# Kernel tuning notes

Hardware: AMD Instinct MI355X
Metric: run time of the kernel (lower is better)

Reference implementation:

```python
import jax, jax.numpy as jnp
import numpy as np

BIG = 1e9      # infinity sentinel used by the CUDA kernels
THRESH = 1e8   # 'min_val >= 1e8 -> invalid' cutoff
MAX_LEN = 512  # init kwarg max_length
BANDWIDTH = 0.2


def _dist(X, Y):
    # pairwise squared-euclidean: D[b,i,j] = sum_d (X[b,i,d]-Y[b,j,d])^2
    diff = X[:, :, None, :] - Y[:, None, :, :]  # [B,N,M,d]
    return jnp.sum(diff * diff, axis=-1)        # [B,N,M]


def _ldtw_dp(D, max_len, bandwidth):
    """Band-limited length-constrained DTW DP.
    Returns (min_vals[B], choices[max_len,B,N,M] int8, best_k[B]).
    choices[t] holds the step-(k=t+1) decisions at interior cells (i-1, j-1)."""
    B, N, M = D.shape
    ii = np.arange(1, N + 1)[:, None]
    jj = np.arange(1, M + 1)[None, :]
    band_bad = jnp.asarray((np.abs(ii - jj) > bandwidth * max(N, M)) & (bandwidth > 0))  # [N,M] static

    # prev_cost padded [B, N+2, M+2]; only (0,0) starts at 0, everything else BIG.
    prev0 = jnp.full((B, N + 2, M + 2), BIG, jnp.float32).at[:, 0, 0].set(0.0)

    def step(prev, _):
        # candidates for interior cells (i in 1..N, j in 1..M)
        cand = jnp.stack(
            [prev[:, 0:N, 0:M],       # diag  (choice 0)
             prev[:, 0:N, 1:M + 1],   # vert  (choice 1)
             prev[:, 1:N + 1, 0:M]],  # hori  (choice 2)
            axis=0)                    # [3,B,N,M]
        min_val = cand.min(axis=0)
        # argmin returns first minimum -> matches strict-less update order (diag,vert,hori)
        choice = jnp.argmin(cand, axis=0).astype(jnp.int8)
        valid = min_val < THRESH
        cost = jnp.where(band_bad[None] | ~valid, BIG, min_val + D)
        ch = jnp.where(valid & ~band_bad[None], choice, jnp.int8(-1))
        curr = jnp.full_like(prev, BIG).at[:, 1:N + 1, 1:M + 1].set(cost)
        return curr, (cost[:, N - 1, M - 1], ch)

    _, (final_costs, choices) = jax.lax.scan(step, prev0, None, length=max_len)
    # final_costs[t] is the cost of a length-(t+1) path ending at (N,M)
    mvl = max(N, M)
    valid_costs = final_costs[mvl - 1:]            # k in [mvl, max_len]
    min_vals = valid_costs.min(axis=0)             # [B]
    best_k = jnp.argmin(valid_costs, axis=0) + mvl # [B] (unused in fwd)
    return min_vals, choices, best_k


def setup_inputs() -> dict:
    key = jax.random.key(0)
    k1, k2 = jax.random.split(key)
    X = jax.random.normal(k1, (16, 256, 64), jnp.float32)
    Y = jax.random.normal(k2, (16, 256, 64), jnp.float32)
    return {"X": X, "Y": Y}


def reference(X, Y):
    D = _dist(X, Y)
    min_vals, _, _ = _ldtw_dp(D, MAX_LEN, BANDWIDTH)
    # original module returns (min_vals, None); the None carries no information
    return min_vals
```

## Files before the change

### kernel.cpp

```cpp
#include <hip/hip_runtime.h>

#define BIGV 1e9f
#define NPT 256

__device__ __forceinline__ int imin_of(int s){
    int a = s - 255; if (a < 0) a = 0;
    int c = s - 50;  c = (c > 0) ? (c >> 1) : 0;
    return (a > c) ? a : c;
}
__device__ __forceinline__ int imax_of(int s){
    int a = (s < 255) ? s : 255;
    int c = (s + 51) >> 1;
    return (a < c) ? a : c;
}

__device__ __forceinline__ int Wof(int g){
    int w = imin_of(8*g + 1) - 1;
    return (w < 0) ? 0 : ((w > 192) ? 192 : w);
}
__device__ __forceinline__ int wrow_of(int s){
    return (s == 0) ? 0 : Wof((s - 1) >> 3);
}

__device__ __forceinline__ float dpp_shr1(float x){
    return __int_as_float(__builtin_amdgcn_update_dpp(
        __float_as_int(BIGV), __float_as_int(x), 0x138 , 0xF, 0xF, false));
}
__device__ __forceinline__ float dpp_shl1(float x){
    return __int_as_float(__builtin_amdgcn_update_dpp(
        __float_as_int(BIGV), __float_as_int(x), 0x130 , 0xF, 0xF, false));
}

__device__ __forceinline__ float min3f(float a, float b, float c){
    float r;
    asm("v_min3_f32 %0, %1, %2, %3" : "=v"(r) : "v"(a), "v"(b), "v"(c));
    return r;
}

__global__ __launch_bounds__(256, 1) void ldtw_dist(const float* __restrict__ X,
                                                    const float* __restrict__ Y,
                                                    float* __restrict__ Dwin)
{
    __shared__ float4 Xs[80*17];
    __shared__ float4 Ys[80*17];
    __shared__ float nX[80], nY[80];
    __shared__ float Band[32*65];
    const int b  = blockIdx.x & 15;
    const int c  = blockIdx.x >> 4;
    const int s0 = c << 5;
    const int s1 = (s0 + 31 > 510) ? 510 : (s0 + 31);
    const int ilo = imin_of(s0), ihi = imax_of(s1);
    const int jlo = s0 - imax_of(s0), jhi = s1 - imin_of(s1);
    const int nx = ihi - ilo + 1, ny = jhi - jlo + 1;
    const int t = threadIdx.x;
    const float4* Xb = (const float4*)(X + (size_t)b * NPT * 64);
    const float4* Yb = (const float4*)(Y + (size_t)b * NPT * 64);

    for (int idx = t; idx < nx * 16; idx += 256){
        int r = idx >> 4, k = idx & 15;
        Xs[r*17 + k] = Xb[(ilo + r)*16 + k];
    }
    for (int idx = t; idx < ny * 16; idx += 256){
        int r = idx >> 4, k = idx & 15;
        Ys[r*17 + k] = Yb[(jlo + r)*16 + k];
    }
    __syncthreads();

    for (int r = t; r < nx + ny; r += 256){
        const float4* row = (r < nx) ? (Xs + r*17) : (Ys + (r - nx)*17);
        float acc = 0.f;
        #pragma unroll
        for (int k = 0; k < 16; ++k){
            float4 v = row[k];
            acc += v.x*v.x + v.y*v.y + v.z*v.z + v.w*v.w;
        }
        if (r < nx) nX[r] = acc; else nY[r - nx] = acc;
    }
    __syncthreads();

    {
        const int ti = t >> 4;
        const int tj = t & 15;
        float acc[5][5];
        #pragma unroll
        for (int u = 0; u < 5; ++u)
            #pragma unroll
            for (int v = 0; v < 5; ++v) acc[u][v] = 0.f;

        #pragma unroll 2
        for (int k = 0; k < 16; ++k){
            float4 xa[5], ya[5];
            #pragma unroll
            for (int u = 0; u < 5; ++u){
                xa[u] = Xs[(ti + u*16)*17 + k];
                ya[u] = Ys[(tj + u*16)*17 + k];
            }
            #pragma unroll
            for (int u = 0; u < 5; ++u)
                #pragma unroll
                for (int v = 0; v < 5; ++v)
                    acc[u][v] += xa[u].x*ya[v].x + xa[u].y*ya[v].y
                               + xa[u].z*ya[v].z + xa[u].w*ya[v].w;
        }

        #pragma unroll
        for (int u = 0; u < 5; ++u){
            #pragma unroll
            for (int v = 0; v < 5; ++v){
                const int iloc = ti + u*16, jloc = tj + v*16;
                const int i = ilo + iloc, j = jlo + jloc;
                const int s = i + j;
                if (s >= s0 && s <= s1){
                    const int im = imin_of(s), ix = imax_of(s);
                    if (i >= im && i <= ix)
                        Band[(s - s0)*65 + (i - im)] =
                            nX[iloc] + nY[jloc] - 2.f*acc[u][v];
                }
            }
        }
    }
    __syncthreads();

    const size_t rowbase = (size_t)(b * 512 + s0) * 64;
    for (int slot = t; slot < 32*64; slot += 256){
        const int sd = slot >> 6, l = slot & 63;
        const int s  = s0 + sd;
        float val = BIGV;
        if (s <= 510){
            const int W = wrow_of(s);
            const int i = W + l;
            const int im = imin_of(s), ix = imax_of(s);
            if (i >= im && i <= ix) val = Band[sd*65 + (i - im)];
        }
        Dwin[rowbase + (size_t)sd*64 + l] = val;
    }
}

__global__ __launch_bounds__(64) void ldtw_dp(const float* __restrict__ Dw,
                                              float* __restrict__ out)
{
    const int b = blockIdx.x;
    const int l = threadIdx.x;
    const float* base = Dw + (size_t)b * 512 * 64 + l;

    float p = base[0];
    float q = BIGV;

#define LOADG(Bk, g) { \
    const float* bp_ = base + (size_t)(8*(g) + 1) * 64; \
    Bk##0 = bp_[0];   Bk##1 = bp_[64];  Bk##2 = bp_[128]; Bk##3 = bp_[192]; \
    Bk##4 = bp_[256]; Bk##5 = bp_[320]; Bk##6 = bp_[384]; Bk##7 = bp_[448]; }

#define SHIFTG(g) { \
    int d_ = Wof(g) - Wof((g) - 1); \
    for (int k_ = 0; k_ < d_; ++k_){ p = dpp_shl1(p); q = dpp_shl1(q); } }

#define STEP_PQ(w) q = min3f(dpp_shr1(p), p, dpp_shr1(q)) + (w);
#define STEP_QP(w) p = min3f(dpp_shr1(q), q, dpp_shr1(p)) + (w);

#define GROUPF(Bk, g) { SHIFTG(g) \
    STEP_PQ(Bk##0) STEP_QP(Bk##1) STEP_PQ(Bk##2) STEP_QP(Bk##3) \
    STEP_PQ(Bk##4) STEP_QP(Bk##5) STEP_PQ(Bk##6) STEP_QP(Bk##7) }

    float A0,A1,A2,A3,A4,A5,A6,A7;
    float B0,B1,B2,B3,B4,B5,B6,B7;
    float C0,C1,C2,C3,C4,C5,C6,C7;
    float E0,E1,E2,E3,E4,E5,E6,E7;
    float F0,F1,F2,F3,F4,F5,F6,F7;
    float G0,G1,G2,G3,G4,G5,G6,G7;
    float H0,H1,H2,H3,H4,H5,H6,H7;
    float K0,K1,K2,K3,K4,K5,K6,K7;

    LOADG(A, 0) LOADG(B, 1) LOADG(C, 2) LOADG(E, 3)
    LOADG(F, 4) LOADG(G, 5) LOADG(H, 6) LOADG(K, 7)

    for (int m = 0; m < 56; m += 8){
        GROUPF(A, m + 0) LOADG(A, m + 8)
        GROUPF(B, m + 1) LOADG(B, m + 9)
        GROUPF(C, m + 2) LOADG(C, m + 10)
        GROUPF(E, m + 3) LOADG(E, m + 11)
        GROUPF(F, m + 4) LOADG(F, m + 12)
        GROUPF(G, m + 5) LOADG(G, m + 13)
        GROUPF(H, m + 6) LOADG(H, m + 14)
        GROUPF(K, m + 7) LOADG(K, m + 15)
    }
    GROUPF(A, 56) GROUPF(B, 57) GROUPF(C, 58) GROUPF(E, 59)
    GROUPF(F, 60) GROUPF(G, 61) GROUPF(H, 62)
    SHIFTG(63)
    STEP_PQ(K0) STEP_QP(K1) STEP_PQ(K2) STEP_QP(K3) STEP_PQ(K4) STEP_QP(K5)

    if (l == 63) out[b] = p;
#undef LOADG
#undef SHIFTG
#undef STEP_PQ
#undef STEP_QP
#undef GROUPF
}

__device__ __forceinline__ float cell_d(const float4* __restrict__ Xb,
                                        const float4* __restrict__ Yb,
                                        int i, int j)
{
    const float4* xr = Xb + i*16;
    const float4* yr = Yb + j*16;
    float acc = 0.f;
    #pragma unroll
    for (int k = 0; k < 16; ++k){
        float4 a = xr[k], bb = yr[k];
        float dx = a.x-bb.x, dy = a.y-bb.y, dz = a.z-bb.z, dw = a.w-bb.w;
        acc += dx*dx + dy*dy + dz*dz + dw*dw;
    }
    return acc;
}

__global__ __launch_bounds__(64) void ldtw_fused_fb(const float* __restrict__ X,
                                                    const float* __restrict__ Y,
                                                    float* __restrict__ out)
{
    const int b = blockIdx.x;
    const int l = threadIdx.x;
    const float4* Xb = (const float4*)(X + (size_t)b * NPT * 64);
    const float4* Yb = (const float4*)(Y + (size_t)b * NPT * 64);
    float prev1 = (l == 0) ? cell_d(Xb, Yb, 0, 0) : BIGV;
    float prev2 = BIGV;
    int base1 = 0, base2 = 0;
    for (int s = 1; s <= 510; ++s){
        const int im = imin_of(s);
        const int ix = imax_of(s);
        const int i  = im + l;
        const bool act = (i <= ix);
        const int ic = act ? i : ix;
        const int j  = s - ic;
        float Dv = cell_d(Xb, Yb, ic, j);
        const int d1 = im - base1, d2 = im - base2;
        float sr1 = dpp_shr1(prev1), sl1 = dpp_shl1(prev1);
        float sr2 = dpp_shr1(prev2), sl2 = dpp_shl1(prev2);
        float m1 = d1 ? fminf(prev1, sl1) : fminf(sr1, prev1);
        float vd = (d2 == 0) ? sr2 : ((d2 == 2) ? sl2 : prev2);
        float m3 = fminf(m1, vd);
        float cur = act ? (m3 + Dv) : BIGV;
        prev2 = prev1; base2 = base1;
        prev1 = cur;   base1 = im;
    }
    if (l == 0) out[b] = prev1;
}

extern "C" void kernel_launch(void* const* d_in, const int* in_sizes, int n_in,
                              void* d_out, int out_size, void* d_ws, size_t ws_size,
                              hipStream_t stream)
{
    const float* X = (const float*)d_in[0];
    const float* Y = (const float*)d_in[1];
    float* out = (float*)d_out;
    const int Bn = in_sizes[0] / (NPT * 64);
    const size_t need = (size_t)Bn * 512 * 64 * 4 + 65536;
    if (ws_size >= need && Bn == 16){
        float* Dwin = (float*)d_ws;
        hipLaunchKernelGGL(ldtw_dist, dim3(256), dim3(256), 0, stream, X, Y, Dwin);
        hipLaunchKernelGGL(ldtw_dp,   dim3(Bn),  dim3(64),  0, stream, Dwin, out);
    } else {
        hipLaunchKernelGGL(ldtw_fused_fb, dim3(Bn), dim3(64), 0, stream, X, Y, out);
    }
}
```

Before: 31.82 us.

## Warp-specialize DP kernel with producer waves staging D windows in LDS

The DP kernel now runs with 256 threads per block. Wave 0 performs the sequential anti-diagonal recurrence while three producer waves copy 64-row chunks of the banded distance window from global memory into a double-buffered LDS array. The compute wave reads its inputs from LDS instead of issuing register-prefetched global loads, which is meant to hide global latency on the serial critical path. In exchange it adds a block-wide barrier every 64 steps and LDS read latency inside the dependency chain.

```diff
diff --git a/kernel.cpp b/kernel.cpp
--- a/kernel.cpp
+++ b/kernel.cpp
@@ -136,20 +136,33 @@
     }
 }
 
-__global__ __launch_bounds__(64) void ldtw_dp(const float* __restrict__ Dw,
-                                              float* __restrict__ out)
-{
-    const int b = blockIdx.x;
-    const int l = threadIdx.x;
-    const float* base = Dw + (size_t)b * 512 * 64 + l;
-
-    float p = base[0];
-    float q = BIGV;
-
-#define LOADG(Bk, g) { \
-    const float* bp_ = base + (size_t)(8*(g) + 1) * 64; \
-    Bk##0 = bp_[0];   Bk##1 = bp_[64];  Bk##2 = bp_[128]; Bk##3 = bp_[192]; \
-    Bk##4 = bp_[256]; Bk##5 = bp_[320]; Bk##6 = bp_[384]; Bk##7 = bp_[448]; }
+__global__ __launch_bounds__(256, 1) void ldtw_dp(const float* __restrict__ Dw,
+                                                  float* __restrict__ out)
+{
+    __shared__ float Dl[2*64*64];
+    const int b  = blockIdx.x;
+    const int t  = threadIdx.x;
+    const int wv = t >> 6;
+    const int l  = t & 63;
+
+    if (wv != 0){
+        const int r = t - 64;
+        const float* src = Dw + ((size_t)b*512 + 1)*64;
+        #pragma unroll
+        for (int k = 0; k < 22; ++k){
+            int idx = r + k*192;
+            if (idx < 4096) Dl[idx] = src[idx];
+        }
+    }
+    float p = BIGV, q = BIGV;
+    if (wv == 0) p = Dw[(size_t)b*512*64 + l];
+    __syncthreads();
+
+#define LOADL(Pr, gi) { \
+    Pr##0 = bufp[((gi)*8 + 0)*64]; Pr##1 = bufp[((gi)*8 + 1)*64]; \
+    Pr##2 = bufp[((gi)*8 + 2)*64]; Pr##3 = bufp[((gi)*8 + 3)*64]; \
+    Pr##4 = bufp[((gi)*8 + 4)*64]; Pr##5 = bufp[((gi)*8 + 5)*64]; \
+    Pr##6 = bufp[((gi)*8 + 6)*64]; Pr##7 = bufp[((gi)*8 + 7)*64]; }
 
 #define SHIFTG(g) { \
     int d_ = Wof(g) - Wof((g) - 1); \
@@ -158,43 +171,52 @@
 #define STEP_PQ(w) q = min3f(dpp_shr1(p), p, dpp_shr1(q)) + (w);
 #define STEP_QP(w) p = min3f(dpp_shr1(q), q, dpp_shr1(p)) + (w);
 
-#define GROUPF(Bk, g) { SHIFTG(g) \
-    STEP_PQ(Bk##0) STEP_QP(Bk##1) STEP_PQ(Bk##2) STEP_QP(Bk##3) \
-    STEP_PQ(Bk##4) STEP_QP(Bk##5) STEP_PQ(Bk##6) STEP_QP(Bk##7) }
-
-    float A0,A1,A2,A3,A4,A5,A6,A7;
-    float B0,B1,B2,B3,B4,B5,B6,B7;
-    float C0,C1,C2,C3,C4,C5,C6,C7;
-    float E0,E1,E2,E3,E4,E5,E6,E7;
-    float F0,F1,F2,F3,F4,F5,F6,F7;
-    float G0,G1,G2,G3,G4,G5,G6,G7;
-    float H0,H1,H2,H3,H4,H5,H6,H7;
-    float K0,K1,K2,K3,K4,K5,K6,K7;
-
-    LOADG(A, 0) LOADG(B, 1) LOADG(C, 2) LOADG(E, 3)
-    LOADG(F, 4) LOADG(G, 5) LOADG(H, 6) LOADG(K, 7)
-
-    for (int m = 0; m < 56; m += 8){
-        GROUPF(A, m + 0) LOADG(A, m + 8)
-        GROUPF(B, m + 1) LOADG(B, m + 9)
-        GROUPF(C, m + 2) LOADG(C, m + 10)
-        GROUPF(E, m + 3) LOADG(E, m + 11)
-        GROUPF(F, m + 4) LOADG(F, m + 12)
-        GROUPF(G, m + 5) LOADG(G, m + 13)
-        GROUPF(H, m + 6) LOADG(H, m + 14)
-        GROUPF(K, m + 7) LOADG(K, m + 15)
-    }
-    GROUPF(A, 56) GROUPF(B, 57) GROUPF(C, 58) GROUPF(E, 59)
-    GROUPF(F, 60) GROUPF(G, 61) GROUPF(H, 62)
-    SHIFTG(63)
-    STEP_PQ(K0) STEP_QP(K1) STEP_PQ(K2) STEP_QP(K3) STEP_PQ(K4) STEP_QP(K5)
-
-    if (l == 63) out[b] = p;
-#undef LOADG
+#define GROUP8C(Pr, g) { SHIFTG(g) \
+    STEP_PQ(Pr##0) STEP_QP(Pr##1) STEP_PQ(Pr##2) STEP_QP(Pr##3) \
+    STEP_PQ(Pr##4) STEP_QP(Pr##5) STEP_PQ(Pr##6) STEP_QP(Pr##7) }
+
+#define GROUP6C(Pr, g) { SHIFTG(g) \
+    STEP_PQ(Pr##0) STEP_QP(Pr##1) STEP_PQ(Pr##2) STEP_QP(Pr##3) \
+    STEP_PQ(Pr##4) STEP_QP(Pr##5) }
+
+    for (int cc = 0; cc < 8; ++cc){
+        if (wv == 0){
+            const float* bufp = Dl + ((cc & 1) << 12) + l;
+            const int g0 = cc << 3;
+            float A0,A1,A2,A3,A4,A5,A6,A7;
+            float B0,B1,B2,B3,B4,B5,B6,B7;
+            LOADL(A, 0)
+            LOADL(B, 1)  GROUP8C(A, g0 + 0)
+            LOADL(A, 2)  GROUP8C(B, g0 + 1)
+            LOADL(B, 3)  GROUP8C(A, g0 + 2)
+            LOADL(A, 4)  GROUP8C(B, g0 + 3)
+            LOADL(B, 5)  GROUP8C(A, g0 + 4)
+            LOADL(A, 6)  GROUP8C(B, g0 + 5)
+            LOADL(B, 7)  GROUP8C(A, g0 + 6)
+            if (cc < 7){ GROUP8C(B, g0 + 7) }
+            else       { GROUP6C(B, 63) }
+        } else if (cc < 7){
+            const int r = t - 64;
+            float* dst = Dl + (((cc + 1) & 1) << 12);
+            const float* src = Dw + ((size_t)b*512 + 64*(cc + 1) + 1)*64;
+            const int lim = (cc == 6) ? 4032 : 4096;
+            #pragma unroll
+            for (int k = 0; k < 22; ++k){
+                int idx = r + k*192;
+                if (idx < lim) dst[idx] = src[idx];
+                else if (idx < 4096) dst[idx] = BIGV;
+            }
+        }
+        __syncthreads();
+    }
+
+    if (t == 63) out[b] = p;
+#undef LOADL
 #undef SHIFTG
 #undef STEP_PQ
 #undef STEP_QP
-#undef GROUPF
+#undef GROUP8C
+#undef GROUP6C
 }
 
 __device__ __forceinline__ float cell_d(const float4* __restrict__ Xb,
@@ -257,7 +279,7 @@
     if (ws_size >= need && Bn == 16){
         float* Dwin = (float*)d_ws;
         hipLaunchKernelGGL(ldtw_dist, dim3(256), dim3(256), 0, stream, X, Y, Dwin);
-        hipLaunchKernelGGL(ldtw_dp,   dim3(Bn),  dim3(64),  0, stream, Dwin, out);
+        hipLaunchKernelGGL(ldtw_dp,   dim3(Bn),  dim3(256), 0, stream, Dwin, out);
     } else {
         hipLaunchKernelGGL(ldtw_fused_fb, dim3(Bn), dim3(64), 0, stream, X, Y, out);
     }
```

New measurement: 32.06 us. About the same (+0.8%).

## Fuse distance and DP kernels into one launch with per-block flag handoff

Applied to the files above, without the earlier changes.

Merges the banded distance kernel and the DP kernel into a single persistent launch. Each block writes its distance tile and publishes a release flag tagged with a magic value plus block id. The first 16 blocks then spin on the 15 other flags for their batch before running the DP. This removes a kernel launch and the inter-kernel gap, but it relies on all 256 blocks being co-resident to avoid deadlock, and the magic-value flags in workspace could match stale values from an earlier call.

```diff
diff --git a/kernel.cpp b/kernel.cpp
--- a/kernel.cpp
+++ b/kernel.cpp
@@ -2,6 +2,7 @@
 
 #define BIGV 1e9f
 #define NPT 256
+#define MAGIC 0x5AD00000u
 
 __device__ __forceinline__ int imin_of(int s){
     int a = s - 255; if (a < 0) a = 0;
@@ -37,22 +38,20 @@
     return r;
 }
 
-__global__ __launch_bounds__(256, 1) void ldtw_dist(const float* __restrict__ X,
-                                                    const float* __restrict__ Y,
-                                                    float* __restrict__ Dwin)
-{
-    __shared__ float4 Xs[80*17];
-    __shared__ float4 Ys[80*17];
-    __shared__ float nX[80], nY[80];
-    __shared__ float Band[32*65];
-    const int b  = blockIdx.x & 15;
-    const int c  = blockIdx.x >> 4;
+__device__ __forceinline__ void dist_phase(const float* __restrict__ X,
+                                           const float* __restrict__ Y,
+                                           float* __restrict__ Dwin,
+                                           int bid, int t,
+                                           float4* Xs, float4* Ys,
+                                           float* nX, float* nY, float* Band)
+{
+    const int b  = bid & 15;
+    const int c  = bid >> 4;
     const int s0 = c << 5;
     const int s1 = (s0 + 31 > 510) ? 510 : (s0 + 31);
     const int ilo = imin_of(s0), ihi = imax_of(s1);
     const int jlo = s0 - imax_of(s0), jhi = s1 - imin_of(s1);
     const int nx = ihi - ilo + 1, ny = jhi - jlo + 1;
-    const int t = threadIdx.x;
     const float4* Xb = (const float4*)(X + (size_t)b * NPT * 64);
     const float4* Yb = (const float4*)(Y + (size_t)b * NPT * 64);
 
@@ -136,11 +135,9 @@
     }
 }
 
-__global__ __launch_bounds__(64) void ldtw_dp(const float* __restrict__ Dw,
-                                              float* __restrict__ out)
-{
-    const int b = blockIdx.x;
-    const int l = threadIdx.x;
+__device__ __forceinline__ void dp_phase(const float* __restrict__ Dw,
+                                         float* __restrict__ out, int b, int l)
+{
     const float* base = Dw + (size_t)b * 512 * 64 + l;
 
     float p = base[0];
@@ -195,6 +192,42 @@
 #undef STEP_PQ
 #undef STEP_QP
 #undef GROUPF
+}
+
+__global__ __launch_bounds__(256, 1) void ldtw_one(const float* __restrict__ X,
+                                                   const float* __restrict__ Y,
+                                                   float* __restrict__ Dwin,
+                                                   unsigned* __restrict__ flags,
+                                                   float* __restrict__ out)
+{
+    __shared__ float4 Xs[80*17];
+    __shared__ float4 Ys[80*17];
+    __shared__ float nX[80], nY[80];
+    __shared__ float Band[32*65];
+
+    const int bid = blockIdx.x;
+    const int t   = threadIdx.x;
+
+    dist_phase(X, Y, Dwin, bid, t, Xs, Ys, nX, nY, Band);
+    __syncthreads();
+    if (t == 0)
+        __hip_atomic_store(&flags[bid], MAGIC + (unsigned)bid,
+                           __ATOMIC_RELEASE, __HIP_MEMORY_SCOPE_AGENT);
+
+    if (bid < 16 && t < 64){
+        const int b = bid, l = t;
+        const bool mine = (l >= 1 && l <= 15);
+        const unsigned* fp = flags + b + (l << 4);
+        const unsigned expect = MAGIC + (unsigned)(b + (l << 4));
+        for (;;){
+            unsigned v = 0u;
+            if (mine)
+                v = __hip_atomic_load(fp, __ATOMIC_RELAXED, __HIP_MEMORY_SCOPE_AGENT);
+            if (__all((int)(!mine || v == expect))) break;
+        }
+        __builtin_amdgcn_fence(__ATOMIC_ACQUIRE, "agent");
+        dp_phase(Dwin, out, b, l);
+    }
 }
 
 __device__ __forceinline__ float cell_d(const float4* __restrict__ Xb,
@@ -253,11 +286,12 @@
     const float* Y = (const float*)d_in[1];
     float* out = (float*)d_out;
     const int Bn = in_sizes[0] / (NPT * 64);
-    const size_t need = (size_t)Bn * 512 * 64 * 4 + 65536;
+    const size_t need = (4u << 20) + 4096;
     if (ws_size >= need && Bn == 16){
         float* Dwin = (float*)d_ws;
-        hipLaunchKernelGGL(ldtw_dist, dim3(256), dim3(256), 0, stream, X, Y, Dwin);
-        hipLaunchKernelGGL(ldtw_dp,   dim3(Bn),  dim3(64),  0, stream, Dwin, out);
+        unsigned* flags = (unsigned*)((char*)d_ws + (4u << 20));
+        hipLaunchKernelGGL(ldtw_one, dim3(256), dim3(256), 0, stream,
+                           X, Y, Dwin, flags, out);
     } else {
         hipLaunchKernelGGL(ldtw_fused_fb, dim3(Bn), dim3(64), 0, stream, X, Y, out);
     }
```

New measurement: 34.21 us. 7.5% more time.
